# Kernel tuning notes

Measured on AMD Instinct MI355X. Metric: run time of the kernel, lower is better.

## Reference

```python
import jax, jax.numpy as jnp
import numpy as np

IN_DIM = 256
OUT_DIM = 256

def setup_inputs() -> dict:
    key = jax.random.key(0)
    k1, k2, k3, k4 = jax.random.split(key, 4)
    B, N, K, D = 4, 10000, 16, IN_DIM
    x = jax.random.normal(k1, (B, N, D), dtype=jnp.float32)
    neigh = jax.random.randint(k2, (N, K), 0, N, dtype=jnp.int64)
    # nn.Linear(2*in_dim, out_dim): W [out, 2*in], b [out]
    bound = 1.0 / np.sqrt(2 * D)
    W = jax.random.uniform(k3, (OUT_DIM, 2 * D), minval=-bound, maxval=bound, dtype=jnp.float32)
    b = jax.random.uniform(k4, (OUT_DIM,), minval=-bound, maxval=bound, dtype=jnp.float32)
    return {"x": x, "neigh": neigh, "W": W, "b": b}

def reference(x, neigh, W, b):
    # x: [B,N,D], neigh: [N,K] with -1 = padding
    mask = (neigh >= 0)                                # [N,K]
    idx = jnp.clip(neigh, 0, None)                     # [N,K]
    # batch_gather_nodes: x_nei[b,n,k,:] = x[b, idx[n,k], :]
    x_nei = x[:, idx, :]                               # [B,N,K,D]
    x_nei = x_nei * mask[None, :, :, None].astype(x.dtype)
    denom = jnp.clip(mask.sum(axis=1), 1, None).astype(x.dtype)  # [N]
    agg = x_nei.sum(axis=2) / denom[None, :, None]     # [B,N,D]
    h = jnp.concatenate([x, agg], axis=-1)             # [B,N,2D]
    return jax.nn.relu(jnp.einsum('bnd,od->bno', h, W) + b)
```

## Files before the change

### kernel.cpp

```cpp
#include <hip/hip_runtime.h>
#include <hip/hip_bf16.h>
#include <stdint.h>

#define B_   4
#define N_   10000
#define K_   16
#define D_   256
#define OUT_ 256
#define KDIM 512
#define M_   (B_ * N_)

#define CH_STRIDE 2056

typedef __attribute__((ext_vector_type(8))) short          short8;
typedef __attribute__((ext_vector_type(8))) unsigned short ushort8;
typedef __attribute__((ext_vector_type(4))) float          f32x4;
typedef __attribute__((ext_vector_type(4))) unsigned short ushort4_t;

__device__ inline unsigned short f2bf(float f) {
    __hip_bfloat16 h = __float2bfloat16(f);
    return *reinterpret_cast<unsigned short*>(&h);
}
__device__ inline float bf2f(unsigned short u) {
    unsigned int v = ((unsigned int)u) << 16;
    return __builtin_bit_cast(float, v);
}

__global__ __launch_bounds__(256) void xprep2(const float* __restrict__ x,
                                              unsigned short* __restrict__ xg) {
    const int t  = threadIdx.x;
    const int n  = blockIdx.x * 2 + (t >> 7);
    const int b  = (t >> 5) & 3;
    const int c0 = (t & 31) * 8;

    const float4* xr = (const float4*)(x + ((size_t)b * N_ + n) * D_ + c0);
    float4 v0 = xr[0];
    float4 v1 = xr[1];
    ushort8 s;
    s[0] = f2bf(v0.x); s[1] = f2bf(v0.y); s[2] = f2bf(v0.z); s[3] = f2bf(v0.w);
    s[4] = f2bf(v1.x); s[5] = f2bf(v1.y); s[6] = f2bf(v1.z); s[7] = f2bf(v1.w);
    *(ushort8*)(xg + ((size_t)n * B_ + b) * D_ + c0) = s;
}

__global__ __launch_bounds__(256) void wconv(const float* __restrict__ W,
                                             unsigned short* __restrict__ Wb) {
    int g = blockIdx.x * 256 + threadIdx.x;
    float4 v = ((const float4*)W)[g];
    ushort4_t s;
    s.x = f2bf(v.x); s.y = f2bf(v.y); s.z = f2bf(v.z); s.w = f2bf(v.w);
    ((ushort4_t*)Wb)[g] = s;
}

__global__ __launch_bounds__(256) void fused_gemm(const unsigned short* __restrict__ xg,
                                                  const int*            __restrict__ neigh,
                                                  const unsigned short* __restrict__ Bm,
                                                  const float*          __restrict__ bias,
                                                  float*                __restrict__ out) {
    __shared__ unsigned short As[16 * CH_STRIDE];
    __shared__ int idx_s[256];

    const int tid = threadIdx.x;
    const int n0  = blockIdx.x * 16;

    idx_s[tid] = neigh[n0 * K_ + tid];
    __syncthreads();

    const int grp = tid >> 5;
    const int gl  = tid & 31;
    const int ch  = gl >> 2;
    const int off = (gl & 3) * 8;

    for (int t = 0; t < 8; ++t) {
        const int ar   = grp * 8 + t;
        const int node = ar >> 2;
        const int b    = ar & 3;

        float acc[8] = {0.f, 0.f, 0.f, 0.f, 0.f, 0.f, 0.f, 0.f};
        int cnt = 0;
#pragma unroll
        for (int k = 0; k < K_; ++k) {
            const int j   = idx_s[node * K_ + k];
            const int jc  = j >= 0 ? j : 0;
            const float m = j >= 0 ? 1.f : 0.f;
            cnt += j >= 0 ? 1 : 0;
            ushort8 v = *(const ushort8*)(xg + (((size_t)jc * B_ + b) << 8) + gl * 8);
#pragma unroll
            for (int e = 0; e < 8; ++e) acc[e] += bf2f(v[e]) * m;
        }
        const float inv = 1.0f / (float)(cnt > 1 ? cnt : 1);

        ushort8 s;
#pragma unroll
        for (int e = 0; e < 8; ++e) s[e] = f2bf(acc[e] * inv);
        *(ushort8*)(As + (8 + ch) * CH_STRIDE + ar * 32 + off) = s;

        ushort8 sv = *(const ushort8*)(xg + (((size_t)(n0 + node) * B_ + b) << 8) + gl * 8);
        *(ushort8*)(As + ch * CH_STRIDE + ar * 32 + off) = sv;
    }
    __syncthreads();

    const int w    = tid >> 6;
    const int lane = tid & 63;
    const int q    = lane >> 4;
    const int r16  = lane & 15;

    f32x4 acc2[4][4] = {};

#pragma unroll 4
    for (int c = 0; c < 16; ++c) {
        short8 a[4], bf[4];
#pragma unroll
        for (int i = 0; i < 4; ++i)
            a[i] = *(const short8*)(As + c * CH_STRIDE + (i * 16 + r16) * 32 + q * 8);
#pragma unroll
        for (int j = 0; j < 4; ++j)
            bf[j] = *(const short8*)(Bm + (size_t)(w * 64 + j * 16 + r16) * KDIM + c * 32 + q * 8);

#pragma unroll
        for (int i = 0; i < 4; ++i)
#pragma unroll
            for (int j = 0; j < 4; ++j)
                acc2[i][j] = __builtin_amdgcn_mfma_f32_16x16x32_bf16(a[i], bf[j], acc2[i][j], 0, 0, 0);
    }

    float bj[4];
#pragma unroll
    for (int j = 0; j < 4; ++j)
        bj[j] = bias[w * 64 + j * 16 + r16];

#pragma unroll
    for (int i = 0; i < 4; ++i) {
#pragma unroll
        for (int reg = 0; reg < 4; ++reg) {
            const int ar = i * 16 + q * 4 + reg;
            const size_t m = (size_t)(ar & 3) * N_ + n0 + (ar >> 2);
            float* orow = out + m * OUT_ + w * 64;
#pragma unroll
            for (int j = 0; j < 4; ++j) {
                float v = acc2[i][j][reg] + bj[j];
                orow[j * 16 + r16] = v > 0.f ? v : 0.f;
            }
        }
    }
}

extern "C" void kernel_launch(void* const* d_in, const int* in_sizes, int n_in,
                              void* d_out, int out_size, void* d_ws, size_t ws_size,
                              hipStream_t stream) {
    const float* x     = (const float*)d_in[0];
    const int*   neigh = (const int*)d_in[1];
    const float* W     = (const float*)d_in[2];
    const float* bias  = (const float*)d_in[3];
    float*       out   = (float*)d_out;

    unsigned short* Wb = (unsigned short*)d_ws;
    unsigned short* xg = Wb + OUT_ * KDIM;

    xprep2<<<N_ / 2, 256, 0, stream>>>(x, xg);
    wconv<<<128, 256, 0, stream>>>(W, Wb);
    fused_gemm<<<N_ / 16, 256, 0, stream>>>(xg, neigh, Wb, bias, out);
}
```

Baseline: 158.6 us.

## Halve GEMM tile rows, batch neighbor loads, and merge prep kernels

Each fused_gemm block now handles 8 nodes (32 rows) instead of 16. This halves LDS use per block and doubles the grid to 1250 blocks, with a launch-bounds hint asking for 4 blocks per CU to raise occupancy. The gather loop issues all 16 neighbor loads up front before accumulating, to expose memory-level parallelism. The x and W bf16 conversion kernels are merged into one launch. In exchange, each block reuses the W tiles over fewer rows, so global/L2 traffic for W doubles, and register pressure from the 16 buffered loads rises.

```diff
diff --git a/kernel.cpp b/kernel.cpp
--- a/kernel.cpp
+++ b/kernel.cpp
@@ -10,7 +10,7 @@
 #define KDIM 512
 #define M_   (B_ * N_)
 
-#define CH_STRIDE 2056
+#define CHS 1032
 
 typedef __attribute__((ext_vector_type(8))) short          short8;
 typedef __attribute__((ext_vector_type(8))) unsigned short ushort8;
@@ -26,76 +26,86 @@
     return __builtin_bit_cast(float, v);
 }
 
-__global__ __launch_bounds__(256) void xprep2(const float* __restrict__ x,
-                                              unsigned short* __restrict__ xg) {
-    const int t  = threadIdx.x;
-    const int n  = blockIdx.x * 2 + (t >> 7);
-    const int b  = (t >> 5) & 3;
-    const int c0 = (t & 31) * 8;
-
-    const float4* xr = (const float4*)(x + ((size_t)b * N_ + n) * D_ + c0);
-    float4 v0 = xr[0];
-    float4 v1 = xr[1];
-    ushort8 s;
-    s[0] = f2bf(v0.x); s[1] = f2bf(v0.y); s[2] = f2bf(v0.z); s[3] = f2bf(v0.w);
-    s[4] = f2bf(v1.x); s[5] = f2bf(v1.y); s[6] = f2bf(v1.z); s[7] = f2bf(v1.w);
-    *(ushort8*)(xg + ((size_t)n * B_ + b) * D_ + c0) = s;
+__global__ __launch_bounds__(256) void prep(const float* __restrict__ x,
+                                            const float* __restrict__ W,
+                                            unsigned short* __restrict__ xg,
+                                            unsigned short* __restrict__ Wb) {
+    const int t = threadIdx.x;
+    if (blockIdx.x < 5000) {
+        const int n  = blockIdx.x * 2 + (t >> 7);
+        const int b  = (t >> 5) & 3;
+        const int c0 = (t & 31) * 8;
+        const float4* xr = (const float4*)(x + ((size_t)b * N_ + n) * D_ + c0);
+        float4 v0 = xr[0];
+        float4 v1 = xr[1];
+        ushort8 s;
+        s[0] = f2bf(v0.x); s[1] = f2bf(v0.y); s[2] = f2bf(v0.z); s[3] = f2bf(v0.w);
+        s[4] = f2bf(v1.x); s[5] = f2bf(v1.y); s[6] = f2bf(v1.z); s[7] = f2bf(v1.w);
+        *(ushort8*)(xg + ((size_t)n * B_ + b) * D_ + c0) = s;
+    } else {
+        int g = (blockIdx.x - 5000) * 256 + t;
+        float4 v = ((const float4*)W)[g];
+        ushort4_t s;
+        s.x = f2bf(v.x); s.y = f2bf(v.y); s.z = f2bf(v.z); s.w = f2bf(v.w);
+        ((ushort4_t*)Wb)[g] = s;
+    }
 }
 
-__global__ __launch_bounds__(256) void wconv(const float* __restrict__ W,
-                                             unsigned short* __restrict__ Wb) {
-    int g = blockIdx.x * 256 + threadIdx.x;
-    float4 v = ((const float4*)W)[g];
-    ushort4_t s;
-    s.x = f2bf(v.x); s.y = f2bf(v.y); s.z = f2bf(v.z); s.w = f2bf(v.w);
-    ((ushort4_t*)Wb)[g] = s;
-}
-
-__global__ __launch_bounds__(256) void fused_gemm(const unsigned short* __restrict__ xg,
-                                                  const int*            __restrict__ neigh,
-                                                  const unsigned short* __restrict__ Bm,
-                                                  const float*          __restrict__ bias,
-                                                  float*                __restrict__ out) {
-    __shared__ unsigned short As[16 * CH_STRIDE];
-    __shared__ int idx_s[256];
+__global__ __launch_bounds__(256, 4) void fused_gemm(const unsigned short* __restrict__ xg,
+                                                     const int*            __restrict__ neigh,
+                                                     const unsigned short* __restrict__ Bm,
+                                                     const float*          __restrict__ bias,
+                                                     float*                __restrict__ out) {
+    __shared__ unsigned short As[16 * CHS];
+    __shared__ int idx_s[8 * K_];
 
     const int tid = threadIdx.x;
-    const int n0  = blockIdx.x * 16;
+    const int n0  = blockIdx.x * 8;
 
-    idx_s[tid] = neigh[n0 * K_ + tid];
+    if (tid < 8 * K_) idx_s[tid] = neigh[n0 * K_ + tid];
     __syncthreads();
 
-    const int grp = tid >> 5;
-    const int gl  = tid & 31;
-    const int ch  = gl >> 2;
-    const int off = (gl & 3) * 8;
-
-    for (int t = 0; t < 8; ++t) {
-        const int ar   = grp * 8 + t;
+#pragma unroll
+    for (int t = 0; t < 4; ++t) {
+        const int task = tid + t * 256;
+        const int ar   = task >> 5;
+        const int seg  = task & 31;
         const int node = ar >> 2;
         const int b    = ar & 3;
 
-        float acc[8] = {0.f, 0.f, 0.f, 0.f, 0.f, 0.f, 0.f, 0.f};
+        int jj[K_];
         int cnt = 0;
 #pragma unroll
         for (int k = 0; k < K_; ++k) {
-            const int j   = idx_s[node * K_ + k];
-            const int jc  = j >= 0 ? j : 0;
-            const float m = j >= 0 ? 1.f : 0.f;
-            cnt += j >= 0 ? 1 : 0;
-            ushort8 v = *(const ushort8*)(xg + (((size_t)jc * B_ + b) << 8) + gl * 8);
+            jj[k] = idx_s[node * K_ + k];
+            cnt += jj[k] >= 0 ? 1 : 0;
+        }
+
+        ushort8 vv[K_];
 #pragma unroll
-            for (int e = 0; e < 8; ++e) acc[e] += bf2f(v[e]) * m;
+        for (int k = 0; k < K_; ++k) {
+            const int jc = jj[k] >= 0 ? jj[k] : 0;
+            vv[k] = *(const ushort8*)(xg + (((size_t)jc * B_ + b) << 8) + seg * 8);
+        }
+        ushort8 sv = *(const ushort8*)(xg + (((size_t)(n0 + node) * B_ + b) << 8) + seg * 8);
+
+        float acc[8] = {0.f, 0.f, 0.f, 0.f, 0.f, 0.f, 0.f, 0.f};
+#pragma unroll
+        for (int k = 0; k < K_; ++k) {
+            const float m = jj[k] >= 0 ? 1.f : 0.f;
+#pragma unroll
+            for (int e = 0; e < 8; ++e) acc[e] += bf2f(vv[k][e]) * m;
         }
         const float inv = 1.0f / (float)(cnt > 1 ? cnt : 1);
 
         ushort8 s;
 #pragma unroll
         for (int e = 0; e < 8; ++e) s[e] = f2bf(acc[e] * inv);
-        *(ushort8*)(As + (8 + ch) * CH_STRIDE + ar * 32 + off) = s;
 
-        ushort8 sv = *(const ushort8*)(xg + (((size_t)(n0 + node) * B_ + b) << 8) + gl * 8);
-        *(ushort8*)(As + ch * CH_STRIDE + ar * 32 + off) = sv;
+        const int ch  = seg >> 2;
+        const int off = (seg & 3) * 8;
+        *(ushort8*)(As + (8 + ch) * CHS + ar * 32 + off) = s;
+        *(ushort8*)(As + ch       * CHS + ar * 32 + off) = sv;
     }
     __syncthreads();
 
@@ -104,20 +114,20 @@
     const int q    = lane >> 4;
     const int r16  = lane & 15;
 
-    f32x4 acc2[4][4] = {};
+    f32x4 acc2[2][4] = {};
 
 #pragma unroll 4
     for (int c = 0; c < 16; ++c) {
-        short8 a[4], bf[4];
+        short8 a[2], bf[4];
 #pragma unroll
-        for (int i = 0; i < 4; ++i)
-            a[i] = *(const short8*)(As + c * CH_STRIDE + (i * 16 + r16) * 32 + q * 8);
+        for (int i = 0; i < 2; ++i)
+            a[i] = *(const short8*)(As + c * CHS + (i * 16 + r16) * 32 + q * 8);
 #pragma unroll
         for (int j = 0; j < 4; ++j)
             bf[j] = *(const short8*)(Bm + (size_t)(w * 64 + j * 16 + r16) * KDIM + c * 32 + q * 8);
 
 #pragma unroll
-        for (int i = 0; i < 4; ++i)
+        for (int i = 0; i < 2; ++i)
 #pragma unroll
             for (int j = 0; j < 4; ++j)
                 acc2[i][j] = __builtin_amdgcn_mfma_f32_16x16x32_bf16(a[i], bf[j], acc2[i][j], 0, 0, 0);
@@ -129,7 +139,7 @@
         bj[j] = bias[w * 64 + j * 16 + r16];
 
 #pragma unroll
-    for (int i = 0; i < 4; ++i) {
+    for (int i = 0; i < 2; ++i) {
 #pragma unroll
         for (int reg = 0; reg < 4; ++reg) {
             const int ar = i * 16 + q * 4 + reg;
@@ -156,7 +166,6 @@
     unsigned short* Wb = (unsigned short*)d_ws;
     unsigned short* xg = Wb + OUT_ * KDIM;
 
-    xprep2<<<N_ / 2, 256, 0, stream>>>(x, xg);
-    wconv<<<128, 256, 0, stream>>>(W, Wb);
-    fused_gemm<<<N_ / 16, 256, 0, stream>>>(xg, neigh, Wb, bias, out);
+    prep<<<5000 + 128, 256, 0, stream>>>(x, W, xg, Wb);
+    fused_gemm<<<N_ / 8, 256, 0, stream>>>(xg, neigh, Wb, bias, out);
 }
```

Result: faster. 154.7 us (-2.4%).
